# Performance work log

Hardware: AMD Instinct MI355X
Metric: run time of the kernel (lower is better)

The kernel has to match this reference:

```python
import jax, jax.numpy as jnp
import numpy as np

M = 23          # number of dendritic subunits
N_SYN = 1500    # number of synapses
T = 30000       # timesteps
B = 101         # temporal kernel length (odd -> 'same' output length)
G_NO = 4        # synapse groups (first half excitatory double-exp kernel)
PAD = B // 2
# parent (1-based) of each subunit; 0 marks root; children have higher index
C_DEN = np.array([0] + [((m - 1) // 2) + 1 for m in range(1, M)], dtype=np.int64)
G_ASSIGN = np.arange(N_SYN, dtype=np.int64) % G_NO   # synapse -> group
SYN_SUB = np.arange(N_SYN, dtype=np.int64) % M       # synapse -> subunit (C_syn nonzeros)


def setup_inputs() -> dict:
    key = jax.random.key(0)
    X = jax.random.uniform(key, (T, N_SYN), dtype=jnp.float32)
    V_o = jnp.ones((1,), jnp.float32) * -69.0
    Tau = jnp.ones((G_NO,), jnp.float32) * 1.4
    Delta = jnp.ones((1,), jnp.float32) * 0.25
    W = jnp.concatenate([jnp.full((G_NO // 2,), 2.0, jnp.float32),
                         jnp.full((G_NO - G_NO // 2,), -1.0, jnp.float32)]) * 0.05
    C = jnp.ones((M,), jnp.float32)
    Theta = jnp.zeros((M,), jnp.float32)
    return {"X": X, "V_o": V_o, "Tau": Tau, "Delta": Delta, "W": W, "C": C, "Theta": Theta}


def _group_kernels(Tau, Delta):
    # shared shifted time base, clamped at 0
    t = jnp.maximum(jnp.arange(B, dtype=jnp.float32) - jnp.exp(Delta[0]), 0.0)  # [B]
    tau = jnp.exp(Tau)[:, None]                               # [G_NO, 1]
    tf = t[None, :] / tau
    fast = tf * jnp.exp(-tf)                                   # alpha kernel
    ts = t[None, :] / (tau * 2.8 + 10.4)
    slow = ts * jnp.exp(-ts) * 0.3
    exc = (fast + slow) / 1.3                                  # dual-exp for excitatory groups
    is_exc = (jnp.arange(G_NO) < G_NO // 2)[:, None]
    return jnp.where(is_exc, exc, fast)                        # [G_NO, B]


def _forward(X, V_o, Tau, Delta, W, C, Theta):
    kern = _group_kernels(Tau, Delta)                          # [G_NO, B]
    g = jnp.asarray(G_ASSIGN)
    # conv is linear, so fold the per-group weight W[g] into the kernel
    k_syn = kern[g] * W[g][:, None]                            # [N_SYN, B]
    # depthwise cross-correlation (matches torch F.conv1d), 'same' padding
    filt = jax.lax.conv_general_dilated(
        X.T[None],                 # [1, N, T]
        k_syn[:, None, :],         # [N, 1, B]
        window_strides=(1,), padding=[(PAD, PAD)],
        feature_group_count=N_SYN,
        dimension_numbers=('NCH', 'OIH', 'NCH'))[0].T          # [T, N]
    # gather-sum of synapses into subunits (C_syn sign only selects membership)
    A = jax.nn.one_hot(jnp.asarray(SYN_SUB), M, dtype=X.dtype)  # [N, M]
    sub_in = filt @ A                                           # [T, M]
    expC = jnp.exp(C)
    # internal nodes processed from leaves toward root (descending indices)
    roots = (np.flip(np.unique(C_DEN))[:-1] - 1).astype(int)
    root_set = set(roots.tolist())
    out = [None] * M
    for m in range(M):                                          # leaves
        if m not in root_set:
            out[m] = jax.nn.sigmoid(sub_in[:, m] - Theta[m]) * expC[m]
    for r in roots:                                             # tree reduction
        s = sub_in[:, r]
        for k in np.where(C_DEN == r + 1)[0]:
            s = s + out[k]
        out[r] = jax.nn.sigmoid(s - Theta[r]) * expC[r]
    return out[0] + V_o[0]                                      # [T]


def reference(X, V_o, Tau, Delta, W, C, Theta):
    return _forward(X, V_o, Tau, Delta, W, C, Theta)
```

## Files before the change

kernel.cpp:

```cpp
#include <hip/hip_runtime.h>
#include <cstddef>

#define T_DIM 30000
#define M_DIM 23
#define NJ    92
#define TILE  64
#define STR   184
#define SUBS  25
#define RROWS 8
#define XP4   377

typedef short bf16x8 __attribute__((ext_vector_type(8)));
typedef float f32x4  __attribute__((ext_vector_type(4)));

__device__ __forceinline__ unsigned short f2bf(float f) {
    unsigned int u = __float_as_uint(f);
    return (unsigned short)((u + 0x7fffu + ((u >> 16) & 1u)) >> 16);
}

__global__ __launch_bounds__(1024) void afrag_k(const float* __restrict__ Tau,
                                                const float* __restrict__ Delta,
                                                const float* __restrict__ W,
                                                unsigned int* __restrict__ afrag) {
    const int tid = threadIdx.x;
    const int f = tid >> 6;
    const int l = tid & 63;
    const int g = f >> 2, kk = f & 3;

    const float eD  = __expf(Delta[0]);
    const float tau = __expf(Tau[g]);
    const float wg  = W[g];

    unsigned short vals[8];
    #pragma unroll
    for (int j = 0; j < 8; ++j) {
        int x = kk * 32 + ((l >> 4) << 3) + j - (l & 15);
        float val = 0.f;
        if (x >= 0 && x <= 100) {
            float tt  = fmaxf((float)x - eD, 0.f);
            float tf  = tt / tau;
            float fast = tf * __expf(-tf);
            float kv;
            if (g < 2) {
                float ts = tt / (tau * 2.8f + 10.4f);
                kv = (fast + ts * __expf(-ts) * 0.3f) * (1.0f / 1.3f);
            } else {
                kv = fast;
            }
            val = kv * wg;
        }
        vals[j] = f2bf(val);
    }
    uint4 o;
    o.x = (unsigned)vals[0] | ((unsigned)vals[1] << 16);
    o.y = (unsigned)vals[2] | ((unsigned)vals[3] << 16);
    o.z = (unsigned)vals[4] | ((unsigned)vals[5] << 16);
    o.w = (unsigned)vals[6] | ((unsigned)vals[7] << 16);
    reinterpret_cast<uint4*>(afrag)[f * 64 + l] = o;
}

__global__ __launch_bounds__(256) void reduce_k(const float* __restrict__ X,
                                                unsigned short* __restrict__ Yb) {
    __shared__ __align__(16) float4 Xs[RROWS * XP4];

    const int tid = threadIdx.x;
    const int tb  = blockIdx.x * RROWS;

    const float4* Xg = reinterpret_cast<const float4*>(X) + (size_t)tb * 375;
    #pragma unroll
    for (int it = 0; it < 12; ++it) {
        int i = tid + 256 * it;
        if (i < 3000) {
            int r = i / 375;
            int pos = i - r * 375;
            Xs[r * XP4 + pos] = Xg[i];
        }
    }
    __syncthreads();

    if (tid < 184) {
        int r = tid / 23;
        int q = tid - 23 * r;
        const float4* row = &Xs[r * XP4];
        float4 s = make_float4(0.f, 0.f, 0.f, 0.f);
        #pragma unroll
        for (int k = 0; k < 16; ++k) {
            float4 v = row[q + 23 * k];
            s.x += v.x; s.y += v.y; s.z += v.z; s.w += v.w;
        }
        if (q < 7) {
            float4 v = row[q + 23 * 16];
            s.x += v.x; s.y += v.y; s.z += v.z; s.w += v.w;
        }
        ushort4 o;
        o.x = f2bf(s.x); o.y = f2bf(s.y); o.z = f2bf(s.z); o.w = f2bf(s.w);
        reinterpret_cast<ushort4*>(Yb)[(size_t)(tb + r) * 23 + q] = o;
    }
}

__global__ __launch_bounds__(512, 4) void conv_tree_k(
    const unsigned short* __restrict__ Yb,
    const unsigned int* __restrict__ afrag,
    const float* __restrict__ Vo,
    const float* __restrict__ C,
    const float* __restrict__ Theta,
    float* __restrict__ out)
{
    __shared__ __align__(16) unsigned short Yt[NJ * STR];
    __shared__ float sub[TILE * SUBS];
    __shared__ float sTheta[M_DIM];
    __shared__ float sExpC[M_DIM];

    const int tid = threadIdx.x;
    const int t0  = blockIdx.x * TILE;

    if (tid < M_DIM) {
        sTheta[tid] = Theta[tid];
        sExpC[tid]  = __expf(C[tid]);
    }

    {
        unsigned int* Yw = reinterpret_cast<unsigned int*>(Yt);
        for (int i = tid; i < 88 * 23; i += 512) {
            int rp = i / 23;
            int q  = i - rp * 23;
            int g0 = t0 - 50 + 2 * rp;
            ushort4 ra = make_ushort4(0, 0, 0, 0);
            ushort4 rb = make_ushort4(0, 0, 0, 0);
            if ((unsigned)g0       < (unsigned)T_DIM) ra = reinterpret_cast<const ushort4*>(Yb)[(size_t)g0 * 23 + q];
            if ((unsigned)(g0 + 1) < (unsigned)T_DIM) rb = reinterpret_cast<const ushort4*>(Yb)[(size_t)(g0 + 1) * 23 + q];
            Yw[(q     ) * 92 + rp] = (unsigned)ra.x | ((unsigned)rb.x << 16);
            Yw[(q + 23) * 92 + rp] = (unsigned)ra.y | ((unsigned)rb.y << 16);
            Yw[(q + 46) * 92 + rp] = (unsigned)ra.z | ((unsigned)rb.z << 16);
            Yw[(q + 69) * 92 + rp] = (unsigned)ra.w | ((unsigned)rb.w << 16);
        }
    }

    const int l    = tid & 63;
    const int wave = tid >> 6;
    const int dt   = (wave & 3) * 16;
    const int nt   = wave >> 2;
    const int n    = l & 15;
    const int m    = nt * 16 + n;
    const bool mvalid = (m < M_DIM);
    const int mc   = mvalid ? m : 0;
    const int kq   = (l >> 4) << 3;

    __syncthreads();

    f32x4 acc = {0.f, 0.f, 0.f, 0.f};
    const uint4* AF = reinterpret_cast<const uint4*>(afrag);

    #pragma unroll
    for (int g = 0; g < 4; ++g) {
        int a  = (3 * ((g - mc) & 3)) & 3;
        int j  = mc + 23 * a;
        int cp = (j >> 2) + 23 * g;
        const unsigned short* colp = &Yt[cp * STR + dt + kq];

        uint4 a0 = AF[(g * 4 + 0) * 64 + l];
        uint4 a1 = AF[(g * 4 + 1) * 64 + l];
        uint4 a2 = AF[(g * 4 + 2) * 64 + l];
        uint4 a3 = AF[(g * 4 + 3) * 64 + l];

        bf16x8 b0 = *reinterpret_cast<const bf16x8*>(colp);
        acc = __builtin_amdgcn_mfma_f32_16x16x32_bf16(__builtin_bit_cast(bf16x8, a0), b0, acc, 0, 0, 0);
        bf16x8 b1 = *reinterpret_cast<const bf16x8*>(colp + 32);
        acc = __builtin_amdgcn_mfma_f32_16x16x32_bf16(__builtin_bit_cast(bf16x8, a1), b1, acc, 0, 0, 0);
        bf16x8 b2 = *reinterpret_cast<const bf16x8*>(colp + 64);
        acc = __builtin_amdgcn_mfma_f32_16x16x32_bf16(__builtin_bit_cast(bf16x8, a2), b2, acc, 0, 0, 0);
        bf16x8 b3 = *reinterpret_cast<const bf16x8*>(colp + 96);
        acc = __builtin_amdgcn_mfma_f32_16x16x32_bf16(__builtin_bit_cast(bf16x8, a3), b3, acc, 0, 0, 0);
    }

    if (mvalid) {
        int i0 = (l >> 4) * 4;
        #pragma unroll
        for (int r = 0; r < 4; ++r)
            sub[(dt + i0 + r) * SUBS + m] = acc[r];
    }
    __syncthreads();

    if (tid < TILE) {
        int t = t0 + tid;
        if (t < T_DIM) {
            const float* s = &sub[tid * SUBS];
            float o[M_DIM];
            #pragma unroll
            for (int mm = 11; mm < 23; ++mm) {
                float x = s[mm] - sTheta[mm];
                o[mm] = sExpC[mm] / (1.f + __expf(-x));
            }
            #pragma unroll
            for (int rr = 10; rr >= 0; --rr) {
                float x = s[rr] + o[2 * rr + 1] + o[2 * rr + 2] - sTheta[rr];
                o[rr] = sExpC[rr] / (1.f + __expf(-x));
            }
            out[t] = o[0] + Vo[0];
        }
    }
}

extern "C" void kernel_launch(void* const* d_in, const int* in_sizes, int n_in,
                              void* d_out, int out_size, void* d_ws, size_t ws_size,
                              hipStream_t stream) {
    const float* X     = (const float*)d_in[0];
    const float* Vo    = (const float*)d_in[1];
    const float* Tau   = (const float*)d_in[2];
    const float* Delta = (const float*)d_in[3];
    const float* W     = (const float*)d_in[4];
    const float* C     = (const float*)d_in[5];
    const float* Theta = (const float*)d_in[6];
    float* out = (float*)d_out;

    unsigned short* Yb = (unsigned short*)d_ws;
    unsigned int* afrag = (unsigned int*)((char*)d_ws + (size_t)T_DIM * NJ * 2);

    afrag_k<<<1, 1024, 0, stream>>>(Tau, Delta, W, afrag);
    reduce_k<<<T_DIM / RROWS, 256, 0, stream>>>(X, Yb);
    conv_tree_k<<<(T_DIM + TILE - 1) / TILE, 512, 0, stream>>>(
        Yb, afrag, Vo, C, Theta, out);
}
```

Baseline: 44.18 us.

## Fuse kernel-fragment setup into reduce kernel and shrink reduce blocks to two rows

Removes the separate single-block afrag_k launch by having block 0 of the reduce kernel also compute the bf16 temporal-kernel fragments. The reduce kernel now handles 2 timestep rows per 128-thread block instead of 8 rows per 256 threads, giving 15000 smaller blocks for more parallelism and less LDS per block. The aim is to cut one launch and improve load balance across CUs. The cost is that only 46 of 128 threads do the summation, and block 0 carries extra serial work.

```diff
diff --git a/kernel.cpp b/kernel.cpp
--- a/kernel.cpp
+++ b/kernel.cpp
@@ -7,7 +7,6 @@
 #define TILE  64
 #define STR   184
 #define SUBS  25
-#define RROWS 8
 #define XP4   377
 
 typedef short bf16x8 __attribute__((ext_vector_type(8)));
@@ -18,67 +17,30 @@
     return (unsigned short)((u + 0x7fffu + ((u >> 16) & 1u)) >> 16);
 }
 
-__global__ __launch_bounds__(1024) void afrag_k(const float* __restrict__ Tau,
+__global__ __launch_bounds__(128) void reduce_k(const float* __restrict__ X,
+                                                const float* __restrict__ Tau,
                                                 const float* __restrict__ Delta,
                                                 const float* __restrict__ W,
+                                                unsigned short* __restrict__ Yb,
                                                 unsigned int* __restrict__ afrag) {
+    __shared__ __align__(16) float4 Xs[2 * XP4];
+
     const int tid = threadIdx.x;
-    const int f = tid >> 6;
-    const int l = tid & 63;
-    const int g = f >> 2, kk = f & 3;
-
-    const float eD  = __expf(Delta[0]);
-    const float tau = __expf(Tau[g]);
-    const float wg  = W[g];
-
-    unsigned short vals[8];
-    #pragma unroll
-    for (int j = 0; j < 8; ++j) {
-        int x = kk * 32 + ((l >> 4) << 3) + j - (l & 15);
-        float val = 0.f;
-        if (x >= 0 && x <= 100) {
-            float tt  = fmaxf((float)x - eD, 0.f);
-            float tf  = tt / tau;
-            float fast = tf * __expf(-tf);
-            float kv;
-            if (g < 2) {
-                float ts = tt / (tau * 2.8f + 10.4f);
-                kv = (fast + ts * __expf(-ts) * 0.3f) * (1.0f / 1.3f);
-            } else {
-                kv = fast;
-            }
-            val = kv * wg;
-        }
-        vals[j] = f2bf(val);
-    }
-    uint4 o;
-    o.x = (unsigned)vals[0] | ((unsigned)vals[1] << 16);
-    o.y = (unsigned)vals[2] | ((unsigned)vals[3] << 16);
-    o.z = (unsigned)vals[4] | ((unsigned)vals[5] << 16);
-    o.w = (unsigned)vals[6] | ((unsigned)vals[7] << 16);
-    reinterpret_cast<uint4*>(afrag)[f * 64 + l] = o;
-}
-
-__global__ __launch_bounds__(256) void reduce_k(const float* __restrict__ X,
-                                                unsigned short* __restrict__ Yb) {
-    __shared__ __align__(16) float4 Xs[RROWS * XP4];
-
-    const int tid = threadIdx.x;
-    const int tb  = blockIdx.x * RROWS;
+    const int tb  = blockIdx.x * 2;
 
     const float4* Xg = reinterpret_cast<const float4*>(X) + (size_t)tb * 375;
     #pragma unroll
-    for (int it = 0; it < 12; ++it) {
-        int i = tid + 256 * it;
-        if (i < 3000) {
-            int r = i / 375;
+    for (int it = 0; it < 6; ++it) {
+        int i = tid + 128 * it;
+        if (i < 750) {
+            int r = (i >= 375) ? 1 : 0;
             int pos = i - r * 375;
             Xs[r * XP4 + pos] = Xg[i];
         }
     }
     __syncthreads();
 
-    if (tid < 184) {
+    if (tid < 46) {
         int r = tid / 23;
         int q = tid - 23 * r;
         const float4* row = &Xs[r * XP4];
@@ -95,6 +57,43 @@
         ushort4 o;
         o.x = f2bf(s.x); o.y = f2bf(s.y); o.z = f2bf(s.z); o.w = f2bf(s.w);
         reinterpret_cast<ushort4*>(Yb)[(size_t)(tb + r) * 23 + q] = o;
+    }
+
+    if (blockIdx.x == 0) {
+        for (int item = tid; item < 1024; item += 128) {
+            int f = item >> 6;
+            int l = item & 63;
+            int g = f >> 2, kk = f & 3;
+            float eD  = __expf(Delta[0]);
+            float tau = __expf(Tau[g]);
+            float wg  = W[g];
+            unsigned short vals[8];
+            #pragma unroll
+            for (int j = 0; j < 8; ++j) {
+                int x = kk * 32 + ((l >> 4) << 3) + j - (l & 15);
+                float val = 0.f;
+                if (x >= 0 && x <= 100) {
+                    float tt  = fmaxf((float)x - eD, 0.f);
+                    float tf  = tt / tau;
+                    float fast = tf * __expf(-tf);
+                    float kv;
+                    if (g < 2) {
+                        float ts = tt / (tau * 2.8f + 10.4f);
+                        kv = (fast + ts * __expf(-ts) * 0.3f) * (1.0f / 1.3f);
+                    } else {
+                        kv = fast;
+                    }
+                    val = kv * wg;
+                }
+                vals[j] = f2bf(val);
+            }
+            uint4 o;
+            o.x = (unsigned)vals[0] | ((unsigned)vals[1] << 16);
+            o.y = (unsigned)vals[2] | ((unsigned)vals[3] << 16);
+            o.z = (unsigned)vals[4] | ((unsigned)vals[5] << 16);
+            o.w = (unsigned)vals[6] | ((unsigned)vals[7] << 16);
+            reinterpret_cast<uint4*>(afrag)[f * 64 + l] = o;
+        }
     }
 }
 
@@ -213,11 +212,10 @@
     const float* Theta = (const float*)d_in[6];
     float* out = (float*)d_out;
 
-    unsigned short* Yb = (unsigned short*)d_ws;
+    unsigned short* Yb  = (unsigned short*)d_ws;
     unsigned int* afrag = (unsigned int*)((char*)d_ws + (size_t)T_DIM * NJ * 2);
 
-    afrag_k<<<1, 1024, 0, stream>>>(Tau, Delta, W, afrag);
-    reduce_k<<<T_DIM / RROWS, 256, 0, stream>>>(X, Yb);
+    reduce_k<<<T_DIM / 2, 128, 0, stream>>>(X, Tau, Delta, W, Yb, afrag);
     conv_tree_k<<<(T_DIM + TILE - 1) / TILE, 512, 0, stream>>>(
         Yb, afrag, Vo, C, Theta, out);
 }
```

Result: faster. 38.34 us (median of 2 runs) (-13.2%).
